# Performance work log

Hardware: AMD Instinct MI355X
Metric: run time of the kernel (lower is better)

The kernel has to match this reference:

```python
import jax, jax.numpy as jnp
import numpy as np

HIDDEN = 1024
HEADS = 16
D_K = HIDDEN // HEADS
NEG_INF = -jnp.inf


def setup_inputs() -> dict:
    key = jax.random.key(0)
    ks = jax.random.split(key, 9)
    N, S = 4, 2048
    scale = 1.0 / np.sqrt(HIDDEN)
    x = jax.random.normal(ks[0], (N, S, HIDDEN), dtype=jnp.float32)
    attn_mask = jnp.ones((N, S), dtype=jnp.int32)
    Wq = jax.random.normal(ks[1], (HIDDEN, HIDDEN), dtype=jnp.float32) * scale
    bq = jnp.zeros((HIDDEN,), dtype=jnp.float32)
    Wk = jax.random.normal(ks[2], (HIDDEN, HIDDEN), dtype=jnp.float32) * scale
    bk = jnp.zeros((HIDDEN,), dtype=jnp.float32)
    Wv = jax.random.normal(ks[3], (HIDDEN, HIDDEN), dtype=jnp.float32) * scale
    bv = jnp.zeros((HIDDEN,), dtype=jnp.float32)
    Wp = jax.random.normal(ks[4], (HIDDEN, HIDDEN), dtype=jnp.float32) * scale
    bp = jnp.zeros((HIDDEN,), dtype=jnp.float32)
    return {"x": x, "attn_mask": attn_mask, "Wq": Wq, "bq": bq,
            "Wk": Wk, "bk": bk, "Wv": Wv, "bv": bv, "Wp": Wp, "bp": bp}


def reference(x, attn_mask, Wq, bq, Wk, bk, Wv, bv, Wp, bp):
    N, S, _ = x.shape
    H, dk = HEADS, D_K
    # torch nn.Linear: y = x @ W.T + b
    q = (x @ Wq.T + bq).reshape(N, S, H, dk).transpose(0, 2, 1, 3)  # (N,H,S,dk)
    k = (x @ Wk.T + bk).reshape(N, S, H, dk).transpose(0, 2, 1, 3)
    v = (x @ Wv.T + bv).reshape(N, S, H, dk).transpose(0, 2, 1, 3)
    attn = jnp.einsum('nhqd,nhkd->nhqk', q, k) / jnp.sqrt(jnp.float32(dk))
    mask = attn_mask.reshape(N, 1, 1, S)
    attn = jnp.where(mask == 0, NEG_INF, attn)
    attn = jax.nn.softmax(attn, axis=-1)
    # dropout is identity in eval mode
    y = jnp.einsum('nhqk,nhkd->nhqd', attn, v)  # (N,H,S,dk)
    y = y.transpose(0, 2, 1, 3).reshape(N, S, H * dk)
    return y @ Wp.T + bp
```

## Files before the change

kernel.cpp:

```cpp
#include <hip/hip_runtime.h>

typedef unsigned short u16;
typedef unsigned int u32;
typedef unsigned long long u64;
typedef __attribute__((ext_vector_type(8))) short bf16x8;
typedef __attribute__((ext_vector_type(4))) short bf16x4;
typedef __attribute__((ext_vector_type(4))) float f32x4;
typedef __attribute__((ext_vector_type(2))) unsigned int u32x2;

#define AS1(p) ((const __attribute__((address_space(1))) void*)(p))
#define AS3(p) ((__attribute__((address_space(3))) void*)(p))

__device__ __forceinline__ u16 f2bf(float f) {
    u32 u = __float_as_uint(f);
    u += 0x7fff + ((u >> 16) & 1);
    return (u16)(u >> 16);
}
__device__ __forceinline__ u32 pack2bf(float lo, float hi) {
    u32 a = __float_as_uint(lo) + 0x8000u;
    u32 b = __float_as_uint(hi) + 0x8000u;
    return __builtin_amdgcn_perm(b, a, 0x07060302);
}
__device__ __forceinline__ u32 cvtpk(float lo, float hi) {
    u32 r;
    asm("v_cvt_pk_bf16_f32 %0, %1, %2" : "=v"(r) : "v"(lo), "v"(hi));
    return r;
}

__device__ __forceinline__ void async16(const u16* g, u16* l) {
    __builtin_amdgcn_global_load_lds(AS1(g), AS3(l), 16, 0, 0);
}

__global__ __launch_bounds__(256) void cvt_kernel(const float* __restrict__ src,
                                                  u16* __restrict__ dst, int n) {
    int idx = (blockIdx.x * 256 + threadIdx.x) * 8;
    if (idx >= n) return;
    float4 a = *(const float4*)(src + idx);
    float4 b = *(const float4*)(src + idx + 4);
    uint4 o;
    o.x = (u32)f2bf(a.x) | ((u32)f2bf(a.y) << 16);
    o.y = (u32)f2bf(a.z) | ((u32)f2bf(a.w) << 16);
    o.z = (u32)f2bf(b.x) | ((u32)f2bf(b.y) << 16);
    o.w = (u32)f2bf(b.z) | ((u32)f2bf(b.w) << 16);
    *(uint4*)(dst + idx) = o;
}

__global__ __launch_bounds__(256) void cvt4_kernel(
    const float* __restrict__ s0, const float* __restrict__ s1,
    const float* __restrict__ s2, const float* __restrict__ s3,
    u16* __restrict__ d0, u16* __restrict__ d1,
    u16* __restrict__ d2, u16* __restrict__ d3) {
    const float* s; u16* d;
    switch (blockIdx.y) {
        case 0:  s = s0; d = d0; break;
        case 1:  s = s1; d = d1; break;
        case 2:  s = s2; d = d2; break;
        default: s = s3; d = d3; break;
    }
    int idx = (blockIdx.x * 256 + threadIdx.x) * 8;
    float4 a = *(const float4*)(s + idx);
    float4 b = *(const float4*)(s + idx + 4);
    uint4 o;
    o.x = (u32)f2bf(a.x) | ((u32)f2bf(a.y) << 16);
    o.y = (u32)f2bf(a.z) | ((u32)f2bf(a.w) << 16);
    o.z = (u32)f2bf(b.x) | ((u32)f2bf(b.y) << 16);
    o.w = (u32)f2bf(b.z) | ((u32)f2bf(b.w) << 16);
    *(uint4*)(d + idx) = o;
}

__global__ __launch_bounds__(256, 2) void gemm_bt(
    const u16* __restrict__ A,
    const u16* __restrict__ Wa, const u16* __restrict__ Wb, const u16* __restrict__ Wc,
    const float* __restrict__ ba, const float* __restrict__ bb, const float* __restrict__ bc,
    void* oa, void* ob_, void* oc, int mode)
{
    constexpr int K = 1024;
    __shared__ u16 smem[32768];

    const int tid = threadIdx.x;
    const int lane = tid & 63, wv = tid >> 6;
    const int l15 = lane & 15, quad = lane >> 4;
    const int wr = wv >> 1, wc = wv & 1;

    const int L = blockIdx.x + (blockIdx.y << 3) + (blockIdx.z << 9);
    const int g = L & 7;
    const int j = L >> 3;
    const int z = j >> 6;
    const int r = j & 63;
    const int m0 = ((g << 3) + (r & 7)) * 128;
    const int n0 = (r >> 3) * 128;

    const u16* W = (z == 0) ? Wa : ((z == 1) ? Wb : Wc);
    const float* bs = (z == 0) ? ba : ((z == 1) ? bb : bc);
    void* out = (z == 0) ? oa : ((z == 1) ? ob_ : oc);
    const bool swap_ = (mode == 1) || (z < 2);

    f32x4 acc[4][4];
#pragma unroll
    for (int i = 0; i < 4; ++i)
#pragma unroll
        for (int j2 = 0; j2 < 4; ++j2) acc[i][j2] = (f32x4)0.f;

    const u16* AsP[4]; const u16* WsP[4]; int offC[4];
#pragma unroll
    for (int jj = 0; jj < 4; ++jj) {
        int c = (wv * 4 + jj) * 64 + lane;
        int row = c >> 3;
        int ko = ((c & 7) ^ (row & 7)) * 8;
        AsP[jj] = A + (size_t)(m0 + row) * K + ko;
        WsP[jj] = W + (size_t)(n0 + row) * K + ko;
        offC[jj] = c * 8;
    }

    auto stage = [&](u16* buf, int kk) {
        u16* At = buf;
        u16* Wt = buf + 8192;
#pragma unroll
        for (int jj = 0; jj < 4; ++jj) async16(AsP[jj] + kk, At + offC[jj]);
#pragma unroll
        for (int jj = 0; jj < 4; ++jj) async16(WsP[jj] + kk, Wt + offC[jj]);
    };
    auto compute = [&](const u16* buf) {
        const u16* At = buf;
        const u16* Wt = buf + 8192;
#pragma unroll
        for (int st = 0; st < 2; ++st) {
            bf16x8 af[4], wf[4];
#pragma unroll
            for (int t = 0; t < 4; ++t) {
                int rowa = wr * 64 + t * 16 + l15;
                af[t] = *(const bf16x8*)&At[rowa * 64 + (((st * 4 + quad) ^ (rowa & 7)) * 8)];
                int rowb = wc * 64 + t * 16 + l15;
                wf[t] = *(const bf16x8*)&Wt[rowb * 64 + (((st * 4 + quad) ^ (rowb & 7)) * 8)];
            }
            __builtin_amdgcn_s_setprio(1);
            if (swap_) {
#pragma unroll
                for (int rt = 0; rt < 4; ++rt)
#pragma unroll
                    for (int ct = 0; ct < 4; ++ct)
                        acc[rt][ct] = __builtin_amdgcn_mfma_f32_16x16x32_bf16(wf[ct], af[rt], acc[rt][ct], 0, 0, 0);
            } else {
#pragma unroll
                for (int rt = 0; rt < 4; ++rt)
#pragma unroll
                    for (int ct = 0; ct < 4; ++ct)
                        acc[rt][ct] = __builtin_amdgcn_mfma_f32_16x16x32_bf16(af[rt], wf[ct], acc[rt][ct], 0, 0, 0);
            }
            __builtin_amdgcn_s_setprio(0);
        }
    };

    u16* const B0 = smem;
    u16* const B1 = smem + 16384;
#define W0 asm volatile("s_waitcnt vmcnt(0)" ::: "memory")
#define BAR __builtin_amdgcn_s_barrier()

    stage(B0, 0);
    W0; BAR;
#pragma unroll 1
    for (int kk = 0; kk < K - 128; kk += 128) {
        stage(B1, kk + 64);  compute(B0); W0; BAR;
        stage(B0, kk + 128); compute(B1); W0; BAR;
    }
    stage(B1, 960); compute(B0); W0; BAR;
    compute(B1);
#undef W0
#undef BAR

    if (mode == 1) {
#pragma unroll
        for (int rt = 0; rt < 4; ++rt)
#pragma unroll
            for (int ct = 0; ct < 4; ++ct) {
                int m_ = m0 + wr * 64 + rt * 16 + l15;
                int ob = n0 + wc * 64 + ct * 16 + quad * 4;
                float4 b4 = *(const float4*)&bs[ob];
                float4 v;
                v.x = acc[rt][ct][0] + b4.x;
                v.y = acc[rt][ct][1] + b4.y;
                v.z = acc[rt][ct][2] + b4.z;
                v.w = acc[rt][ct][3] + b4.w;
                *(float4*)((float*)out + (size_t)m_ * 1024 + ob) = v;
            }
        return;
    }

    __syncthreads();

    const int n = m0 >> 11, s0 = m0 & 2047;
    if (z < 2) {
        const float qs = (z == 0) ? 0.18033688011112042f : 1.0f;
#pragma unroll
        for (int rt = 0; rt < 4; ++rt)
#pragma unroll
            for (int ct = 0; ct < 4; ++ct) {
                int ml = wr * 64 + rt * 16 + l15;
                int ol = wc * 64 + ct * 16 + quad * 4;
                float4 b4 = *(const float4*)&bs[n0 + ol];
                float v0 = (acc[rt][ct][0] + b4.x) * qs;
                float v1 = (acc[rt][ct][1] + b4.y) * qs;
                float v2 = (acc[rt][ct][2] + b4.z) * qs;
                float v3 = (acc[rt][ct][3] + b4.w) * qs;
                u32x2 pv = { pack2bf(v0, v1), pack2bf(v2, v3) };
                *(u32x2*)&smem[ml * 132 + ol] = pv;
            }
        __syncthreads();
        const int h0 = n0 >> 6;
#pragma unroll
        for (int p = 0; p < 8; ++p) {
            int hh = p >> 2, qq = p & 3;
            int m = qq * 32 + (tid >> 3), d = (tid & 7) * 8;
            bf16x8 vv = *(const bf16x8*)&smem[m * 132 + hh * 64 + d];
            u16* dst = (u16*)out + ((size_t)((n * 16 + h0 + hh) * 2048 + s0 + m)) * 64 + d;
            *(bf16x8*)dst = vv;
        }
    } else {
#pragma unroll
        for (int rt = 0; rt < 4; ++rt)
#pragma unroll
            for (int ct = 0; ct < 4; ++ct) {
                int ol = wc * 64 + ct * 16 + l15;
                int ml = wr * 64 + rt * 16 + quad * 4;
                float b = bs[n0 + ol];
                float v0 = acc[rt][ct][0] + b;
                float v1 = acc[rt][ct][1] + b;
                float v2 = acc[rt][ct][2] + b;
                float v3 = acc[rt][ct][3] + b;
                u32x2 pv = { pack2bf(v0, v1), pack2bf(v2, v3) };
                *(u32x2*)&smem[ol * 132 + ml] = pv;
            }
        __syncthreads();
#pragma unroll
        for (int p = 0; p < 8; ++p) {
            int o = p * 16 + (tid >> 4), ms = (tid & 15) * 8;
            bf16x8 vv = *(const bf16x8*)&smem[o * 132 + ms];
            int og = n0 + o;
            int h = og >> 6, d = og & 63;
            u16* dst = (u16*)out + ((size_t)((n * 16 + h) * 64 + d)) * 2048 + s0 + ms;
            *(bf16x8*)dst = vv;
        }
    }
}

__global__ __launch_bounds__(256, 2) void attn_kernel(
    const u16* __restrict__ Q, const u16* __restrict__ K_,
    const u16* __restrict__ VT, const int* __restrict__ mask,
    u16* __restrict__ Y)
{
    constexpr int S = 2048, DK = 64, STR = 72;
    __shared__ u16 Kt[2][64 * STR];
    __shared__ u16 Vt[2][64 * STR];

    const int tid = threadIdx.x;
    const int lane = tid & 63, w = tid >> 6;
    const int l15 = lane & 15, quad = lane >> 4;

    const int L = blockIdx.x + (blockIdx.y << 3);
    const int vb = (L & 7) * 64 + (L >> 3);
    const int nh = vb >> 3;
    const int n = nh >> 4, h = nh & 15;
    const int qbase = (vb & 7) * 256;

    const u16* Qh = Q + (size_t)nh * S * DK;
    const u16* Kh = K_ + (size_t)nh * S * DK;
    const u16* Vh = VT + (size_t)nh * DK * S;

    bf16x8 qf[4][2];
#pragma unroll
    for (int nt = 0; nt < 4; ++nt)
#pragma unroll
        for (int st = 0; st < 2; ++st)
            qf[nt][st] = *(const bf16x8*)(Qh + (size_t)(qbase + w * 64 + nt * 16 + l15) * DK + st * 32 + quad * 8);

    f32x4 o[4][4];
#pragma unroll
    for (int dt = 0; dt < 4; ++dt)
#pragma unroll
        for (int nt = 0; nt < 4; ++nt) o[dt][nt] = (f32x4)0.f;
    float lsum[4] = {0.f, 0.f, 0.f, 0.f};

    const int r0 = tid >> 3, c8 = (tid & 7) * 8;

    u32 bm = 0;
    for (int t = 0; t < 32; ++t) {
        int mv = mask[n * S + t * 64 + lane];
        if (__ballot(mv != 0) == ~0ull) bm |= (1u << t);
    }

    {
        bf16x8 k0 = *(const bf16x8*)(Kh + (size_t)r0 * 64 + c8);
        bf16x8 k1 = *(const bf16x8*)(Kh + (size_t)(r0 + 32) * 64 + c8);
        bf16x8 v0 = *(const bf16x8*)(Vh + (size_t)r0 * S + c8);
        bf16x8 v1 = *(const bf16x8*)(Vh + (size_t)(r0 + 32) * S + c8);
        *(bf16x8*)&Kt[0][r0 * STR + c8] = k0;
        *(bf16x8*)&Kt[0][(r0 + 32) * STR + c8] = k1;
        *(bf16x8*)&Vt[0][r0 * STR + c8] = v0;
        *(bf16x8*)&Vt[0][(r0 + 32) * STR + c8] = v1;
    }
    __syncthreads();

    const f32x4 zf = (f32x4)0.f;

#define QK_JT(jt) do {                                                                       \
    bf16x8 kf0_ = *(const bf16x8*)&Ktc[((jt) * 16 + l15) * STR + quad * 8];                  \
    bf16x8 kf1_ = *(const bf16x8*)&Ktc[((jt) * 16 + l15) * STR + 32 + quad * 8];             \
    _Pragma("unroll")                                                                        \
    for (int nt = 0; nt < 4; ++nt) {                                                         \
        sacc[jt][nt] = __builtin_amdgcn_mfma_f32_16x16x32_bf16(kf0_, qf[nt][0], zf, 0, 0, 0);\
        sacc[jt][nt] = __builtin_amdgcn_mfma_f32_16x16x32_bf16(kf1_, qf[nt][1], sacc[jt][nt], 0, 0, 0);\
    }                                                                                        \
} while (0)

#define SM_JT(jt) do {                                                                       \
    if (!fast) {                                                                             \
        _Pragma("unroll")                                                                    \
        for (int rr = 0; rr < 4; ++rr) {                                                     \
            int mv_ = mask[n * S + it * 64 + (jt) * 16 + quad * 4 + rr];                     \
            _Pragma("unroll")                                                                \
            for (int nt = 0; nt < 4; ++nt)                                                   \
                if (mv_ == 0) sacc[jt][nt][rr] = -1e30f;                                     \
        }                                                                                    \
    }                                                                                        \
    _Pragma("unroll")                                                                        \
    for (int nt = 0; nt < 4; ++nt) {                                                         \
        float e0_ = __builtin_amdgcn_exp2f(sacc[jt][nt][0]);                                 \
        float e1_ = __builtin_amdgcn_exp2f(sacc[jt][nt][1]);                                 \
        float e2_ = __builtin_amdgcn_exp2f(sacc[jt][nt][2]);                                 \
        float e3_ = __builtin_amdgcn_exp2f(sacc[jt][nt][3]);                                 \
        ps[nt] += (e0_ + e1_) + (e2_ + e3_);                                                 \
        pkx[nt][jt] = cvtpk(e0_, e1_);                               \
        pky[nt][jt] = cvtpk(e2_, e3_);                               \
    }                                                                                        \
} while (0)

#define PB_KT(kt) do {                                                                       \
    _Pragma("unroll")                                                                        \
    for (int nt = 0; nt < 4; ++nt) {                                                         \
        auto rX_ = __builtin_amdgcn_permlane32_swap(pkx[nt][2 * (kt)], pkx[nt][2 * (kt) + 1], false, false);\
        auto rY_ = __builtin_amdgcn_permlane32_swap(pky[nt][2 * (kt)], pky[nt][2 * (kt) + 1], false, false);\
        auto sX_ = __builtin_amdgcn_permlane16_swap(rX_[0], rX_[1], false, false);           \
        auto sY_ = __builtin_amdgcn_permlane16_swap(rY_[0], rY_[1], false, false);           \
        union { u32 u[4]; bf16x8 v; } pu_;                                                   \
        pu_.u[0] = sX_[0];                                           \
        pu_.u[1] = sY_[0];                                                       \
        pu_.u[2] = sX_[1];                                                       \
        pu_.u[3] = sY_[1];                                                       \
        pb[nt] = pu_.v;                                                                      \
    }                                                                                        \
} while (0)

#define PV_KT(kt) do {                                                                       \
    _Pragma("unroll")                                                                        \
    for (int dt = 0; dt < 4; ++dt) {                                                         \
        bf16x8 vf_ = *(const bf16x8*)&Vtc[(dt * 16 + l15) * STR + (kt) * 32 + quad * 8];     \
        _Pragma("unroll")                                                                    \
        for (int nt = 0; nt < 4; ++nt)                                                       \
            o[dt][nt] = __builtin_amdgcn_mfma_f32_16x16x32_bf16(vf_, pb[nt], o[dt][nt], 0, 0, 0);\
    }                                                                                        \
} while (0)

#pragma unroll 1
    for (int it = 0; it < 32; ++it) {
        const int cur = it & 1, nxt = cur ^ 1;
        const u16* Ktc = &Kt[cur][0];
        const u16* Vtc = &Vt[cur][0];
        const bool fast = (bm >> it) & 1;

        const int kkn = ((it + 1) << 6) & (S - 1);
        bf16x8 rk0 = *(const bf16x8*)(Kh + (size_t)(kkn + r0) * 64 + c8);
        bf16x8 rk1 = *(const bf16x8*)(Kh + (size_t)(kkn + r0 + 32) * 64 + c8);
        bf16x8 rv0 = *(const bf16x8*)(Vh + (size_t)r0 * S + kkn + c8);
        bf16x8 rv1 = *(const bf16x8*)(Vh + (size_t)(r0 + 32) * S + kkn + c8);

        f32x4 sacc[4][4];
        u32 pkx[4][4], pky[4][4];
        float ps[4] = {0.f, 0.f, 0.f, 0.f};
        bf16x8 pb[4];

        __builtin_amdgcn_s_setprio(1);
        QK_JT(0);
        QK_JT(1);
        SM_JT(0);
        QK_JT(2);
        SM_JT(1);
        QK_JT(3);
        SM_JT(2);
        PB_KT(0);
        PV_KT(0);
        SM_JT(3);
        PB_KT(1);
        *(bf16x8*)&Kt[nxt][r0 * STR + c8] = rk0;
        *(bf16x8*)&Kt[nxt][(r0 + 32) * STR + c8] = rk1;
        *(bf16x8*)&Vt[nxt][r0 * STR + c8] = rv0;
        *(bf16x8*)&Vt[nxt][(r0 + 32) * STR + c8] = rv1;
        PV_KT(1);
        __builtin_amdgcn_s_setprio(0);

#pragma unroll
        for (int nt = 0; nt < 4; ++nt) lsum[nt] += ps[nt];

        __syncthreads();
    }
#undef QK_JT
#undef SM_JT
#undef PB_KT
#undef PV_KT

#pragma unroll
    for (int nt = 0; nt < 4; ++nt) {
        float ls = lsum[nt];
        ls += __shfl_xor(ls, 16);
        ls += __shfl_xor(ls, 32);
        float rl = (ls > 0.f) ? 1.f / ls : 0.f;
        int qi = qbase + w * 64 + nt * 16 + l15;
#pragma unroll
        for (int dt = 0; dt < 4; ++dt) {
            u32x2 pv = { pack2bf(o[dt][nt][0] * rl, o[dt][nt][1] * rl),
                         pack2bf(o[dt][nt][2] * rl, o[dt][nt][3] * rl) };
            size_t base = ((size_t)(n * 2048 + qi)) * 1024 + h * 64 + dt * 16 + quad * 4;
            *(u32x2*)(Y + base) = pv;
        }
    }
}

extern "C" void kernel_launch(void* const* d_in, const int* in_sizes, int n_in,
                              void* d_out, int out_size, void* d_ws, size_t ws_size,
                              hipStream_t stream) {
    const float* x  = (const float*)d_in[0];
    const int* mask = (const int*)d_in[1];
    const float* Wq = (const float*)d_in[2];
    const float* bq = (const float*)d_in[3];
    const float* Wk = (const float*)d_in[4];
    const float* bk = (const float*)d_in[5];
    const float* Wv = (const float*)d_in[6];
    const float* bv = (const float*)d_in[7];
    const float* Wp = (const float*)d_in[8];
    const float* bp = (const float*)d_in[9];

    char* ws = (char*)d_ws;
    u16* xb  = (u16*)(ws);
    u16* wqb = (u16*)(ws + (16u << 20));
    u16* wkb = (u16*)(ws + (18u << 20));
    u16* wvb = (u16*)(ws + (20u << 20));
    u16* wpb = (u16*)(ws + (22u << 20));
    u16* Qb  = (u16*)(ws + (24u << 20));
    u16* Kb  = (u16*)(ws + (40u << 20));
    u16* Vb  = (u16*)(ws + (56u << 20));
    u16* Yb  = (u16*)(ws + (72u << 20));

    cvt_kernel<<<4096, 256, 0, stream>>>(x, xb, 8388608);
    cvt4_kernel<<<dim3(512, 4), 256, 0, stream>>>(Wq, Wk, Wv, Wp, wqb, wkb, wvb, wpb);

    gemm_bt<<<dim3(8, 64, 3), 256, 0, stream>>>(xb, wqb, wkb, wvb, bq, bk, bv,
                                                (void*)Qb, (void*)Kb, (void*)Vb, 0);

    attn_kernel<<<dim3(8, 64), 256, 0, stream>>>(Qb, Kb, Vb, mask, Yb);

    gemm_bt<<<dim3(8, 64, 1), 256, 0, stream>>>(Yb, wpb, wpb, wpb, bp, bp, bp,
                                                d_out, d_out, d_out, 1);
}
```

Baseline: 261.4 us.

## Use 8 waves and triple-buffered LDS pipeline in projection GEMM

The projection GEMM block grows from 4 to 8 waves, each computing a 32x64 sub-tile instead of 64x64, which halves per-thread accumulators and staging loads. The LDS double buffer becomes a three-buffer ring with prefetch distance two, waiting with vmcnt(4) so one stage's loads stay in flight during compute. LDS use rises to 96 KB per block, which may limit how many blocks fit per CU, and each wave now re-reads the W fragments for a smaller M slice.

```diff
diff --git a/kernel.cpp b/kernel.cpp
--- a/kernel.cpp
+++ b/kernel.cpp
@@ -68,19 +68,19 @@
     *(uint4*)(d + idx) = o;
 }
 
-__global__ __launch_bounds__(256, 2) void gemm_bt(
+__global__ __launch_bounds__(512, 2) void gemm_bt(
     const u16* __restrict__ A,
     const u16* __restrict__ Wa, const u16* __restrict__ Wb, const u16* __restrict__ Wc,
     const float* __restrict__ ba, const float* __restrict__ bb, const float* __restrict__ bc,
     void* oa, void* ob_, void* oc, int mode)
 {
     constexpr int K = 1024;
-    __shared__ u16 smem[32768];
+    __shared__ u16 smem[49152];
 
     const int tid = threadIdx.x;
     const int lane = tid & 63, wv = tid >> 6;
     const int l15 = lane & 15, quad = lane >> 4;
-    const int wr = wv >> 1, wc = wv & 1;
+    const int wm = wv >> 1, wn = wv & 1;
 
     const int L = blockIdx.x + (blockIdx.y << 3) + (blockIdx.z << 9);
     const int g = L & 7;
@@ -95,16 +95,16 @@
     void* out = (z == 0) ? oa : ((z == 1) ? ob_ : oc);
     const bool swap_ = (mode == 1) || (z < 2);
 
-    f32x4 acc[4][4];
-#pragma unroll
-    for (int i = 0; i < 4; ++i)
+    f32x4 acc[2][4];
+#pragma unroll
+    for (int i = 0; i < 2; ++i)
 #pragma unroll
         for (int j2 = 0; j2 < 4; ++j2) acc[i][j2] = (f32x4)0.f;
 
-    const u16* AsP[4]; const u16* WsP[4]; int offC[4];
-#pragma unroll
-    for (int jj = 0; jj < 4; ++jj) {
-        int c = (wv * 4 + jj) * 64 + lane;
+    const u16* AsP[2]; const u16* WsP[2]; int offC[2];
+#pragma unroll
+    for (int jj = 0; jj < 2; ++jj) {
+        int c = jj * 512 + tid;
         int row = c >> 3;
         int ko = ((c & 7) ^ (row & 7)) * 8;
         AsP[jj] = A + (size_t)(m0 + row) * K + ko;
@@ -116,33 +116,37 @@
         u16* At = buf;
         u16* Wt = buf + 8192;
 #pragma unroll
-        for (int jj = 0; jj < 4; ++jj) async16(AsP[jj] + kk, At + offC[jj]);
-#pragma unroll
-        for (int jj = 0; jj < 4; ++jj) async16(WsP[jj] + kk, Wt + offC[jj]);
+        for (int jj = 0; jj < 2; ++jj) {
+            async16(AsP[jj] + kk, At + offC[jj]);
+            async16(WsP[jj] + kk, Wt + offC[jj]);
+        }
     };
     auto compute = [&](const u16* buf) {
         const u16* At = buf;
         const u16* Wt = buf + 8192;
 #pragma unroll
         for (int st = 0; st < 2; ++st) {
-            bf16x8 af[4], wf[4];
+            bf16x8 af[2], wf[4];
+#pragma unroll
+            for (int t = 0; t < 2; ++t) {
+                int rowa = wm * 32 + t * 16 + l15;
+                af[t] = *(const bf16x8*)&At[rowa * 64 + (((st * 4 + quad) ^ (rowa & 7)) * 8)];
+            }
 #pragma unroll
             for (int t = 0; t < 4; ++t) {
-                int rowa = wr * 64 + t * 16 + l15;
-                af[t] = *(const bf16x8*)&At[rowa * 64 + (((st * 4 + quad) ^ (rowa & 7)) * 8)];
-                int rowb = wc * 64 + t * 16 + l15;
+                int rowb = wn * 64 + t * 16 + l15;
                 wf[t] = *(const bf16x8*)&Wt[rowb * 64 + (((st * 4 + quad) ^ (rowb & 7)) * 8)];
             }
             __builtin_amdgcn_s_setprio(1);
             if (swap_) {
 #pragma unroll
-                for (int rt = 0; rt < 4; ++rt)
+                for (int rt = 0; rt < 2; ++rt)
 #pragma unroll
                     for (int ct = 0; ct < 4; ++ct)
                         acc[rt][ct] = __builtin_amdgcn_mfma_f32_16x16x32_bf16(wf[ct], af[rt], acc[rt][ct], 0, 0, 0);
             } else {
 #pragma unroll
-                for (int rt = 0; rt < 4; ++rt)
+                for (int rt = 0; rt < 2; ++rt)
 #pragma unroll
                     for (int ct = 0; ct < 4; ++ct)
                         acc[rt][ct] = __builtin_amdgcn_mfma_f32_16x16x32_bf16(af[rt], wf[ct], acc[rt][ct], 0, 0, 0);
@@ -151,30 +155,39 @@
         }
     };
 
-    u16* const B0 = smem;
-    u16* const B1 = smem + 16384;
+#define W4 asm volatile("s_waitcnt vmcnt(4)" ::: "memory")
 #define W0 asm volatile("s_waitcnt vmcnt(0)" ::: "memory")
 #define BAR __builtin_amdgcn_s_barrier()
 
-    stage(B0, 0);
+    u16* pc = smem;
+    u16* pn = smem + 16384;
+    u16* ps = smem + 32768;
+
+    stage(pc, 0);
+    stage(pn, 64);
+    W4; BAR;
+#pragma unroll 1
+    for (int t = 0; t < 14; ++t) {
+        stage(ps, 128 + t * 64);
+        compute(pc);
+        W4; BAR;
+        u16* tmp = pc; pc = pn; pn = ps; ps = tmp;
+    }
+    compute(pc);
     W0; BAR;
-#pragma unroll 1
-    for (int kk = 0; kk < K - 128; kk += 128) {
-        stage(B1, kk + 64);  compute(B0); W0; BAR;
-        stage(B0, kk + 128); compute(B1); W0; BAR;
-    }
-    stage(B1, 960); compute(B0); W0; BAR;
-    compute(B1);
+    pc = pn;
+    compute(pc);
+#undef W4
 #undef W0
 #undef BAR
 
     if (mode == 1) {
 #pragma unroll
-        for (int rt = 0; rt < 4; ++rt)
+        for (int rt = 0; rt < 2; ++rt)
 #pragma unroll
             for (int ct = 0; ct < 4; ++ct) {
-                int m_ = m0 + wr * 64 + rt * 16 + l15;
-                int ob = n0 + wc * 64 + ct * 16 + quad * 4;
+                int m_ = m0 + wm * 32 + rt * 16 + l15;
+                int ob = n0 + wn * 64 + ct * 16 + quad * 4;
                 float4 b4 = *(const float4*)&bs[ob];
                 float4 v;
                 v.x = acc[rt][ct][0] + b4.x;
@@ -192,11 +205,11 @@
     if (z < 2) {
         const float qs = (z == 0) ? 0.18033688011112042f : 1.0f;
 #pragma unroll
-        for (int rt = 0; rt < 4; ++rt)
+        for (int rt = 0; rt < 2; ++rt)
 #pragma unroll
             for (int ct = 0; ct < 4; ++ct) {
-                int ml = wr * 64 + rt * 16 + l15;
-                int ol = wc * 64 + ct * 16 + quad * 4;
+                int ml = wm * 32 + rt * 16 + l15;
+                int ol = wn * 64 + ct * 16 + quad * 4;
                 float4 b4 = *(const float4*)&bs[n0 + ol];
                 float v0 = (acc[rt][ct][0] + b4.x) * qs;
                 float v1 = (acc[rt][ct][1] + b4.y) * qs;
@@ -208,20 +221,20 @@
         __syncthreads();
         const int h0 = n0 >> 6;
 #pragma unroll
-        for (int p = 0; p < 8; ++p) {
-            int hh = p >> 2, qq = p & 3;
-            int m = qq * 32 + (tid >> 3), d = (tid & 7) * 8;
+        for (int p = 0; p < 4; ++p) {
+            int hh = p >> 1, mh = p & 1;
+            int m = mh * 64 + (tid >> 3), d = (tid & 7) * 8;
             bf16x8 vv = *(const bf16x8*)&smem[m * 132 + hh * 64 + d];
             u16* dst = (u16*)out + ((size_t)((n * 16 + h0 + hh) * 2048 + s0 + m)) * 64 + d;
             *(bf16x8*)dst = vv;
         }
     } else {
 #pragma unroll
-        for (int rt = 0; rt < 4; ++rt)
+        for (int rt = 0; rt < 2; ++rt)
 #pragma unroll
             for (int ct = 0; ct < 4; ++ct) {
-                int ol = wc * 64 + ct * 16 + l15;
-                int ml = wr * 64 + rt * 16 + quad * 4;
+                int ol = wn * 64 + ct * 16 + l15;
+                int ml = wm * 32 + rt * 16 + quad * 4;
                 float b = bs[n0 + ol];
                 float v0 = acc[rt][ct][0] + b;
                 float v1 = acc[rt][ct][1] + b;
@@ -232,8 +245,8 @@
             }
         __syncthreads();
 #pragma unroll
-        for (int p = 0; p < 8; ++p) {
-            int o = p * 16 + (tid >> 4), ms = (tid & 15) * 8;
+        for (int p = 0; p < 4; ++p) {
+            int o = p * 32 + (tid >> 4), ms = (tid & 15) * 8;
             bf16x8 vv = *(const bf16x8*)&smem[o * 132 + ms];
             int og = n0 + o;
             int h = og >> 6, d = og & 63;
@@ -452,11 +465,11 @@
     cvt_kernel<<<4096, 256, 0, stream>>>(x, xb, 8388608);
     cvt4_kernel<<<dim3(512, 4), 256, 0, stream>>>(Wq, Wk, Wv, Wp, wqb, wkb, wvb, wpb);
 
-    gemm_bt<<<dim3(8, 64, 3), 256, 0, stream>>>(xb, wqb, wkb, wvb, bq, bk, bv,
+    gemm_bt<<<dim3(8, 64, 3), 512, 0, stream>>>(xb, wqb, wkb, wvb, bq, bk, bv,
                                                 (void*)Qb, (void*)Kb, (void*)Vb, 0);
 
     attn_kernel<<<dim3(8, 64), 256, 0, stream>>>(Qb, Kb, Vb, mask, Yb);
 
-    gemm_bt<<<dim3(8, 64, 1), 256, 0, stream>>>(Yb, wpb, wpb, wpb, bp, bp, bp,
+    gemm_bt<<<dim3(8, 64, 1), 512, 0, stream>>>(Yb, wpb, wpb, wpb, bp, bp, bp,
                                                 d_out, d_out, d_out, 1);
 }
```

Result: slower. 268.9 us (+2.9%).
